# Kernel optimization log

Measured on AMD Instinct MI355X. Metric: run time of the kernel, lower is better.

The kernel has to match this reference:

```python
import jax, jax.numpy as jnp
import numpy as np

EMBED_DIM = 1024
NUM_HEADS = 16
HEAD_DIM = EMBED_DIM // NUM_HEADS
B, S = 4, 2048


def setup_inputs() -> dict:
    key = jax.random.key(0)
    ks = jax.random.split(key, 9)
    scale = 1.0 / np.sqrt(EMBED_DIM)
    x = jax.random.normal(ks[0], (B, S, EMBED_DIM), dtype=jnp.float32)
    Wq = jax.random.normal(ks[1], (EMBED_DIM, EMBED_DIM), dtype=jnp.float32) * scale
    Wk = jax.random.normal(ks[2], (EMBED_DIM, EMBED_DIM), dtype=jnp.float32) * scale
    Wv = jax.random.normal(ks[3], (EMBED_DIM, EMBED_DIM), dtype=jnp.float32) * scale
    Wo = jax.random.normal(ks[4], (EMBED_DIM, EMBED_DIM), dtype=jnp.float32) * scale
    bq = jnp.zeros((EMBED_DIM,), jnp.float32)
    bk = jnp.zeros((EMBED_DIM,), jnp.float32)
    bv = jnp.zeros((EMBED_DIM,), jnp.float32)
    bo = jnp.zeros((EMBED_DIM,), jnp.float32)
    return {"x": x, "Wq": Wq, "bq": bq, "Wk": Wk, "bk": bk, "Wv": Wv, "bv": bv, "Wo": Wo, "bo": bo}


def _split_heads(t):
    # [B,S,E] -> [B,H,S,D]
    b, s, _ = t.shape
    return t.reshape(b, s, NUM_HEADS, HEAD_DIM).transpose(0, 2, 1, 3)


def reference(x, Wq, bq, Wk, bk, Wv, bv, Wo, bo):
    q = _split_heads(x @ Wq + bq)
    k = _split_heads(x @ Wk + bk)
    v = _split_heads(x @ Wv + bv)
    scale = 1.0 / jnp.sqrt(jnp.asarray(HEAD_DIM, x.dtype))
    scores = jnp.einsum('bhqd,bhkd->bhqk', q, k) * scale  # [B,H,S,S]
    weights = jax.nn.softmax(scores, axis=-1)
    attn = jnp.einsum('bhqk,bhkd->bhqd', weights, v)  # [B,H,S,D]
    b, h, s, d = attn.shape
    concat = attn.transpose(0, 2, 1, 3).reshape(b, s, h * d)
    return concat @ Wo + bo
```

## Files before the change

### kernel.cpp

```cpp
#include <hip/hip_runtime.h>
#include <hip/hip_bf16.h>

typedef unsigned short u16;
typedef __attribute__((ext_vector_type(8))) short bf16x8;
typedef __attribute__((ext_vector_type(4))) float f32x4;
typedef __attribute__((ext_vector_type(4))) unsigned short u16x4;

#define EMB 1024
#define SEQ 2048
#define NH 16
#define HD 64

#define OFF_WT   0u
#define OFF_WOT  3145728u
#define OFF_Q    4194304u
#define OFF_K    12582912u
#define OFF_VT   20971520u
#define OFF_OC   29360128u

#define QSCALE 0.1803368801111f

__device__ __forceinline__ u16 f2bf(float f) {
    unsigned int x; __builtin_memcpy(&x, &f, 4);
    unsigned int r = x + 0x7fffu + ((x >> 16) & 1u);
    return (u16)(r >> 16);
}

#if defined(__has_builtin) && __has_builtin(__builtin_amdgcn_cvt_pk_bf16_f32)
typedef __attribute__((ext_vector_type(2))) __bf16 bfv2;
__device__ __forceinline__ unsigned int pkbf(float a, float b) {
    bfv2 v = __builtin_amdgcn_cvt_pk_bf16_f32(a, b);
    unsigned int u; __builtin_memcpy(&u, &v, 4); return u;
}
#else
__device__ __forceinline__ unsigned int pkbf(float a, float b) {
    return (unsigned)f2bf(a) | ((unsigned)f2bf(b) << 16);
}
#endif

#if defined(__has_builtin) && __has_builtin(__builtin_amdgcn_exp2f)
__device__ __forceinline__ float exp2fast(float x) { return __builtin_amdgcn_exp2f(x); }
#else
__device__ __forceinline__ float exp2fast(float x) { return __builtin_exp2f(x); }
#endif

__device__ __forceinline__ void gld_lds16(const void* gsrc, void* ldst) {
    void* g = const_cast<void*>(gsrc);
    __builtin_amdgcn_global_load_lds((__attribute__((address_space(1))) void*)g,
                                     (__attribute__((address_space(3))) void*)ldst,
                                     16, 0, 0);
}

__global__ __launch_bounds__(256) void convert_x(
    const float* __restrict__ x, u16* __restrict__ xb)
{
    int i = (blockIdx.x * 256 + threadIdx.x) * 4;
    float4 v = *(const float4*)&x[i];
    uint2 o = { pkbf(v.x, v.y), pkbf(v.z, v.w) };
    *(uint2*)&xb[i] = o;
}

__global__ __launch_bounds__(256) void transpose_w(
    const float* __restrict__ W0, const float* __restrict__ W1,
    const float* __restrict__ W2, const float* __restrict__ W3,
    u16* __restrict__ ws)
{
    __shared__ u16 tile[64 * 65];
    const float* src = blockIdx.z == 0 ? W0 : blockIdx.z == 1 ? W1 : blockIdx.z == 2 ? W2 : W3;
    u16* dst = ws + (blockIdx.z < 3 ? (unsigned)blockIdx.z * 1048576u : OFF_WOT);
    const int k0 = blockIdx.x * 64, n0 = blockIdx.y * 64;
    const int t = threadIdx.x;
    #pragma unroll
    for (int i = 0; i < 16; i++) {
        int idx = i * 256 + t; int r = idx >> 6, c = idx & 63;
        tile[c * 65 + r] = f2bf(src[(k0 + r) * EMB + n0 + c]);
    }
    __syncthreads();
    #pragma unroll
    for (int i = 0; i < 16; i++) {
        int idx = i * 256 + t; int r = idx >> 6, c = idx & 63;
        dst[(n0 + r) * EMB + k0 + c] = tile[r * 65 + c];
    }
}

__global__ __launch_bounds__(256) void gemm_qkv(
    const u16* __restrict__ X, const u16* __restrict__ WT,
    const float* __restrict__ bq, const float* __restrict__ bk, const float* __restrict__ bv,
    u16* __restrict__ Qt, u16* __restrict__ Ko, u16* __restrict__ Vt)
{
    __shared__ u16 Al[128 * 32];
    __shared__ u16 Bl[128 * 32];
    const int t = threadIdx.x, lane = t & 63, w = t >> 6;
    const int quad = lane >> 4, l15 = lane & 15;
    const int wr = w >> 1, wc = w & 1;
    const int m0 = blockIdx.x * 128, n0 = blockIdx.y * 128;
    const f32x4 fzero = {0.f, 0.f, 0.f, 0.f};

    f32x4 acc[4][4];
    #pragma unroll
    for (int i = 0; i < 4; i++)
        #pragma unroll
        for (int j = 0; j < 4; j++) acc[i][j] = fzero;

    for (int kt = 0; kt < 32; ++kt) {
        #pragma unroll
        for (int r = 0; r < 2; r++) {
            int g = r * 256 + t; int row = g >> 2, cw = g & 3;
            int sc = (cw ^ ((row >> 1) & 3)) * 8;
            gld_lds16(X  + (size_t)(m0 + row) * EMB + kt * 32 + sc, &Al[g * 8]);
            gld_lds16(WT + (size_t)(n0 + row) * EMB + kt * 32 + sc, &Bl[g * 8]);
        }
        __syncthreads();
        bf16x8 af[4], bfr[4];
        #pragma unroll
        for (int i = 0; i < 4; i++) {
            int rowA = wr * 64 + i * 16 + l15;
            af[i] = *(const bf16x8*)&Al[rowA * 32 + ((quad ^ ((rowA >> 1) & 3)) * 8)];
        }
        #pragma unroll
        for (int j = 0; j < 4; j++) {
            int rowB = wc * 64 + j * 16 + l15;
            bfr[j] = *(const bf16x8*)&Bl[rowB * 32 + ((quad ^ ((rowB >> 1) & 3)) * 8)];
        }
        #pragma unroll
        for (int i = 0; i < 4; i++)
            #pragma unroll
            for (int j = 0; j < 4; j++)
                acc[i][j] = __builtin_amdgcn_mfma_f32_16x16x32_bf16(af[i], bfr[j], acc[i][j], 0, 0, 0);
        __syncthreads();
    }

    const int seg = n0 >> 10;
    const float* bias = seg == 0 ? bq : (seg == 1 ? bk : bv);
    #pragma unroll
    for (int j = 0; j < 4; j++) {
        int n = n0 + wc * 64 + j * 16 + l15;
        int nn = n & 1023;
        float bvl = bias[nn];
        int h = nn >> 6, d = nn & 63;
        #pragma unroll
        for (int i = 0; i < 4; i++) {
            int m = m0 + wr * 64 + i * 16 + quad * 4;
            int b = m >> 11, s = m & 2047;
            if (seg == 0) {
                uint2 pp = { pkbf((acc[i][j][0] + bvl) * QSCALE, (acc[i][j][1] + bvl) * QSCALE),
                             pkbf((acc[i][j][2] + bvl) * QSCALE, (acc[i][j][3] + bvl) * QSCALE) };
                *(uint2*)&Qt[(size_t)((b * NH + h) * HD + d) * SEQ + s] = pp;
            } else if (seg == 2) {
                uint2 pp = { pkbf(acc[i][j][0] + bvl, acc[i][j][1] + bvl),
                             pkbf(acc[i][j][2] + bvl, acc[i][j][3] + bvl) };
                *(uint2*)&Vt[(size_t)((b * NH + h) * HD + d) * SEQ + s] = pp;
            } else {
                size_t base = (size_t)((b * NH + h) * SEQ + s) * HD + d;
                #pragma unroll
                for (int r = 0; r < 4; r++) Ko[base + (size_t)r * HD] = f2bf(acc[i][j][r] + bvl);
            }
        }
    }
}

__global__ __launch_bounds__(256, 2) void flash_attn(
    const u16* __restrict__ Q, const u16* __restrict__ K,
    const u16* __restrict__ VT, u16* __restrict__ Oc)
{
    __shared__ u16 Kl[64 * 64];
    __shared__ u16 Vl[64 * 64];
    __shared__ u16 Pl[4 * 64 * 72];
    const int t = threadIdx.x, lane = t & 63, w = t >> 6;
    const int quad = lane >> 4, l15 = lane & 15;
    const int a7 = l15 & 7;
    const int bh = blockIdx.y;
    const int b = bh >> 4, h = bh & 15;
    const int q0 = blockIdx.x * 256 + w * 64;
    const u16* Qtb = Q + (size_t)bh * HD * SEQ;
    const u16* Kb  = K + (size_t)bh * SEQ * HD;
    const u16* Vb  = VT + (size_t)bh * HD * SEQ;
    const f32x4 fzero = {0.f, 0.f, 0.f, 0.f};

    const u16* kbase0 = &Kl[l15 * 64 + ((quad ^ a7) * 8)];
    const u16* kbase1 = &Kl[l15 * 64 + (((4 + quad) ^ a7) * 8)];
    const u16* vbase0 = &Vl[l15 * 64 + ((quad ^ a7) * 8)];
    const u16* vbase1 = &Vl[l15 * 64 + (((4 + quad) ^ a7) * 8)];
    u16* Pw = &Pl[w * 64 * 72];
    u16* pww = Pw + l15 * 72 + quad * 4;
    const u16* pwr = Pw + l15 * 72 + quad * 8;

    bf16x8 ones;
    #pragma unroll
    for (int j = 0; j < 8; j++) ones[j] = (short)0x3F80;

    bf16x8 qf[4][2];
    #pragma unroll
    for (int i = 0; i < 4; i++)
        #pragma unroll
        for (int c = 0; c < 2; c++)
            #pragma unroll
            for (int j = 0; j < 8; j++)
                qf[i][c][j] = (short)Qtb[(size_t)(c * 32 + quad * 8 + j) * SEQ + q0 + i * 16 + l15];

    f32x4 oacc[4][4];
    f32x4 oextra[4];
    #pragma unroll
    for (int i = 0; i < 4; i++) {
        oextra[i] = fzero;
        #pragma unroll
        for (int f = 0; f < 4; f++) oacc[i][f] = fzero;
    }

    for (int kt = 0; kt < 32; ++kt) {
        #pragma unroll
        for (int r = 0; r < 2; r++) {
            int g = r * 256 + t, row = g >> 3, cw = g & 7;
            int swz = (cw ^ (row & 7)) * 8;
            gld_lds16(Kb + (size_t)kt * 64 * HD + row * HD + swz, &Kl[g * 8]);
            gld_lds16(Vb + (size_t)row * SEQ + kt * 64 + swz, &Vl[g * 8]);
        }
        __syncthreads();

        {
            bf16x8 ak[2][4];
            #pragma unroll
            for (int f = 0; f < 4; f++) {
                ak[0][f] = *(const bf16x8*)(kbase0 + f * 1024);
                ak[1][f] = *(const bf16x8*)(kbase1 + f * 1024);
            }
            #pragma unroll
            for (int i = 0; i < 4; i++) {
                f32x4 sf[4];
                #pragma unroll
                for (int f = 0; f < 4; f++) sf[f] = fzero;
                #pragma unroll
                for (int c = 0; c < 2; c++)
                    #pragma unroll
                    for (int f = 0; f < 4; f++)
                        sf[f] = __builtin_amdgcn_mfma_f32_16x16x32_bf16(ak[c][f], qf[i][c], sf[f], 0, 0, 0);
                #pragma unroll
                for (int f = 0; f < 4; f++) {
                    float p0 = exp2fast(sf[f][0]);
                    float p1 = exp2fast(sf[f][1]);
                    float p2 = exp2fast(sf[f][2]);
                    float p3 = exp2fast(sf[f][3]);
                    uint2 pp = { pkbf(p0, p1), pkbf(p2, p3) };
                    *(uint2*)(pww + i * 1152 + f * 16) = pp;
                }
            }
        }

        {
            bf16x8 av[2][4];
            #pragma unroll
            for (int f = 0; f < 4; f++) {
                av[0][f] = *(const bf16x8*)(vbase0 + f * 1024);
                av[1][f] = *(const bf16x8*)(vbase1 + f * 1024);
            }
            #pragma unroll
            for (int i = 0; i < 4; i++) {
                bf16x8 bp0 = *(const bf16x8*)(pwr + i * 1152);
                bf16x8 bp1 = *(const bf16x8*)(pwr + i * 1152 + 32);
                #pragma unroll
                for (int f = 0; f < 4; f++) {
                    oacc[i][f] = __builtin_amdgcn_mfma_f32_16x16x32_bf16(av[0][f], bp0, oacc[i][f], 0, 0, 0);
                    oacc[i][f] = __builtin_amdgcn_mfma_f32_16x16x32_bf16(av[1][f], bp1, oacc[i][f], 0, 0, 0);
                }
                oextra[i] = __builtin_amdgcn_mfma_f32_16x16x32_bf16(ones, bp0, oextra[i], 0, 0, 0);
                oextra[i] = __builtin_amdgcn_mfma_f32_16x16x32_bf16(ones, bp1, oextra[i], 0, 0, 0);
            }
        }
        __syncthreads();
    }

    #pragma unroll
    for (int i = 0; i < 4; i++) {
        float inv = 1.0f / oextra[i][0];
        int s = q0 + i * 16 + l15;
        size_t base = ((size_t)(b * SEQ + s) * NH + h) * HD;
        #pragma unroll
        for (int f = 0; f < 4; f++) {
            uint2 o = { pkbf(oacc[i][f][0] * inv, oacc[i][f][1] * inv),
                        pkbf(oacc[i][f][2] * inv, oacc[i][f][3] * inv) };
            *(uint2*)&Oc[base + f * 16 + quad * 4] = o;
        }
    }
}

__global__ __launch_bounds__(256) void gemm_out(
    const u16* __restrict__ A, const u16* __restrict__ WT,
    const float* __restrict__ bo, float* __restrict__ out)
{
    __shared__ u16 Al[128 * 32];
    __shared__ u16 Bl[128 * 32];
    const int t = threadIdx.x, lane = t & 63, w = t >> 6;
    const int quad = lane >> 4, l15 = lane & 15;
    const int wr = w >> 1, wc = w & 1;
    const int m0 = blockIdx.x * 128, n0 = blockIdx.y * 128;
    const f32x4 fzero = {0.f, 0.f, 0.f, 0.f};

    f32x4 acc[4][4];
    #pragma unroll
    for (int i = 0; i < 4; i++)
        #pragma unroll
        for (int j = 0; j < 4; j++) acc[i][j] = fzero;

    for (int kt = 0; kt < 32; ++kt) {
        #pragma unroll
        for (int r = 0; r < 2; r++) {
            int g = r * 256 + t; int row = g >> 2, cw = g & 3;
            int sc = (cw ^ ((row >> 1) & 3)) * 8;
            gld_lds16(A  + (size_t)(m0 + row) * EMB + kt * 32 + sc, &Al[g * 8]);
            gld_lds16(WT + (size_t)(n0 + row) * EMB + kt * 32 + sc, &Bl[g * 8]);
        }
        __syncthreads();
        bf16x8 af[4], bfr[4];
        #pragma unroll
        for (int i = 0; i < 4; i++) {
            int rowA = wr * 64 + i * 16 + l15;
            af[i] = *(const bf16x8*)&Al[rowA * 32 + ((quad ^ ((rowA >> 1) & 3)) * 8)];
        }
        #pragma unroll
        for (int j = 0; j < 4; j++) {
            int rowB = wc * 64 + j * 16 + l15;
            bfr[j] = *(const bf16x8*)&Bl[rowB * 32 + ((quad ^ ((rowB >> 1) & 3)) * 8)];
        }
        #pragma unroll
        for (int i = 0; i < 4; i++)
            #pragma unroll
            for (int j = 0; j < 4; j++)
                acc[i][j] = __builtin_amdgcn_mfma_f32_16x16x32_bf16(af[i], bfr[j], acc[i][j], 0, 0, 0);
        __syncthreads();
    }

    #pragma unroll
    for (int j = 0; j < 4; j++) {
        int n = n0 + wc * 64 + j * 16 + l15;
        float bvl = bo[n];
        #pragma unroll
        for (int i = 0; i < 4; i++) {
            int m = m0 + wr * 64 + i * 16 + quad * 4;
            #pragma unroll
            for (int r = 0; r < 4; r++)
                out[(size_t)(m + r) * EMB + n] = acc[i][j][r] + bvl;
        }
    }
}

extern "C" void kernel_launch(void* const* d_in, const int* in_sizes, int n_in,
                              void* d_out, int out_size, void* d_ws, size_t ws_size,
                              hipStream_t stream)
{
    (void)in_sizes; (void)n_in; (void)out_size; (void)ws_size;
    const float* x  = (const float*)d_in[0];
    const float* Wq = (const float*)d_in[1];
    const float* bq = (const float*)d_in[2];
    const float* Wk = (const float*)d_in[3];
    const float* bk = (const float*)d_in[4];
    const float* Wv = (const float*)d_in[5];
    const float* bv = (const float*)d_in[6];
    const float* Wo = (const float*)d_in[7];
    const float* bo = (const float*)d_in[8];
    u16* ws = (u16*)d_ws;
    u16* Xb = (u16*)d_out;

    convert_x<<<dim3(8192), 256, 0, stream>>>(x, Xb);
    transpose_w<<<dim3(16, 16, 4), 256, 0, stream>>>(Wq, Wk, Wv, Wo, ws);
    gemm_qkv<<<dim3(64, 24), 256, 0, stream>>>(Xb, ws + OFF_WT, bq, bk, bv,
                                               ws + OFF_Q, ws + OFF_K, ws + OFF_VT);
    flash_attn<<<dim3(8, 64), 256, 0, stream>>>(ws + OFF_Q, ws + OFF_K,
                                                ws + OFF_VT, ws + OFF_OC);
    gemm_out<<<dim3(64, 8), 256, 0, stream>>>(ws + OFF_OC, ws + OFF_WOT, bo, (float*)d_out);
}
```

Measured before the change: 292.6 us.

## Double-buffer K/V tiles and interleave QK/PV per row block in flash attention

The flash attention loop now prefetches the next K/V tile into a second LDS buffer while computing on the current one. It uses a single barrier per iteration instead of loading and then syncing. The QK^T, exp and PV steps are fused per 16-row block, with a small P scratch buffer that alternates by parity, and s_setprio raises wave priority around the MFMA groups. This is meant to hide global-load latency and cut LDS footprint. In exchange it needs more registers, since av and ak are both live, and LDS use for K/V doubles.

Result: no change. 295.9 us (+1.1%).

```diff
diff --git a/kernel.cpp b/kernel.cpp
--- a/kernel.cpp
+++ b/kernel.cpp
@@ -163,9 +163,9 @@
     const u16* __restrict__ Q, const u16* __restrict__ K,
     const u16* __restrict__ VT, u16* __restrict__ Oc)
 {
-    __shared__ u16 Kl[64 * 64];
-    __shared__ u16 Vl[64 * 64];
-    __shared__ u16 Pl[4 * 64 * 72];
+    __shared__ u16 Kl[2][64 * 64];
+    __shared__ u16 Vl[2][64 * 64];
+    __shared__ u16 Pl[4][2][16 * 72];
     const int t = threadIdx.x, lane = t & 63, w = t >> 6;
     const int quad = lane >> 4, l15 = lane & 15;
     const int a7 = l15 & 7;
@@ -177,13 +177,10 @@
     const u16* Vb  = VT + (size_t)bh * HD * SEQ;
     const f32x4 fzero = {0.f, 0.f, 0.f, 0.f};
 
-    const u16* kbase0 = &Kl[l15 * 64 + ((quad ^ a7) * 8)];
-    const u16* kbase1 = &Kl[l15 * 64 + (((4 + quad) ^ a7) * 8)];
-    const u16* vbase0 = &Vl[l15 * 64 + ((quad ^ a7) * 8)];
-    const u16* vbase1 = &Vl[l15 * 64 + (((4 + quad) ^ a7) * 8)];
-    u16* Pw = &Pl[w * 64 * 72];
-    u16* pww = Pw + l15 * 72 + quad * 4;
-    const u16* pwr = Pw + l15 * 72 + quad * 8;
+    const int kf0 = l15 * 64 + ((quad ^ a7) * 8);
+    const int kf1 = l15 * 64 + (((4 + quad) ^ a7) * 8);
+    u16* pww = &Pl[w][0][l15 * 72 + quad * 4];
+    const u16* pwr = &Pl[w][0][l15 * 72 + quad * 8];
 
     bf16x8 ones;
     #pragma unroll
@@ -207,66 +204,79 @@
         for (int f = 0; f < 4; f++) oacc[i][f] = fzero;
     }
 
-    for (int kt = 0; kt < 32; ++kt) {
+    auto stage = [&](int kt, int bsel) {
         #pragma unroll
         for (int r = 0; r < 2; r++) {
             int g = r * 256 + t, row = g >> 3, cw = g & 7;
             int swz = (cw ^ (row & 7)) * 8;
-            gld_lds16(Kb + (size_t)kt * 64 * HD + row * HD + swz, &Kl[g * 8]);
-            gld_lds16(Vb + (size_t)row * SEQ + kt * 64 + swz, &Vl[g * 8]);
-        }
-        __syncthreads();
-
-        {
-            bf16x8 ak[2][4];
+            gld_lds16(Kb + (size_t)kt * 64 * HD + row * HD + swz, &Kl[bsel][g * 8]);
+            gld_lds16(Vb + (size_t)row * SEQ + kt * 64 + swz, &Vl[bsel][g * 8]);
+        }
+    };
+
+    stage(0, 0);
+    asm volatile("s_waitcnt vmcnt(0) lgkmcnt(0)" ::: "memory");
+    __builtin_amdgcn_s_barrier();
+    __builtin_amdgcn_sched_barrier(0);
+
+    int cur = 0;
+    for (int kt = 0; kt < 32; ++kt) {
+        if (kt < 31) stage(kt + 1, cur ^ 1);
+
+        const u16* kbuf = &Kl[cur][0];
+        const u16* vbuf = &Vl[cur][0];
+        bf16x8 ak[2][4], av[2][4];
+        #pragma unroll
+        for (int f = 0; f < 4; f++) {
+            ak[0][f] = *(const bf16x8*)(kbuf + kf0 + f * 1024);
+            ak[1][f] = *(const bf16x8*)(kbuf + kf1 + f * 1024);
+            av[0][f] = *(const bf16x8*)(vbuf + kf0 + f * 1024);
+            av[1][f] = *(const bf16x8*)(vbuf + kf1 + f * 1024);
+        }
+
+        #pragma unroll
+        for (int i = 0; i < 4; i++) {
+            const int par = (i & 1) * 1152;
+            f32x4 sf[4];
+            #pragma unroll
+            for (int f = 0; f < 4; f++) sf[f] = fzero;
+            __builtin_amdgcn_s_setprio(1);
+            #pragma unroll
+            for (int c = 0; c < 2; c++)
+                #pragma unroll
+                for (int f = 0; f < 4; f++)
+                    sf[f] = __builtin_amdgcn_mfma_f32_16x16x32_bf16(ak[c][f], qf[i][c], sf[f], 0, 0, 0);
+            __builtin_amdgcn_s_setprio(0);
+
             #pragma unroll
             for (int f = 0; f < 4; f++) {
-                ak[0][f] = *(const bf16x8*)(kbase0 + f * 1024);
-                ak[1][f] = *(const bf16x8*)(kbase1 + f * 1024);
+                float p0 = exp2fast(sf[f][0]);
+                float p1 = exp2fast(sf[f][1]);
+                float p2 = exp2fast(sf[f][2]);
+                float p3 = exp2fast(sf[f][3]);
+                uint2 pp = { pkbf(p0, p1), pkbf(p2, p3) };
+                *(uint2*)(pww + par + f * 16) = pp;
             }
-            #pragma unroll
-            for (int i = 0; i < 4; i++) {
-                f32x4 sf[4];
-                #pragma unroll
-                for (int f = 0; f < 4; f++) sf[f] = fzero;
-                #pragma unroll
-                for (int c = 0; c < 2; c++)
-                    #pragma unroll
-                    for (int f = 0; f < 4; f++)
-                        sf[f] = __builtin_amdgcn_mfma_f32_16x16x32_bf16(ak[c][f], qf[i][c], sf[f], 0, 0, 0);
-                #pragma unroll
-                for (int f = 0; f < 4; f++) {
-                    float p0 = exp2fast(sf[f][0]);
-                    float p1 = exp2fast(sf[f][1]);
-                    float p2 = exp2fast(sf[f][2]);
-                    float p3 = exp2fast(sf[f][3]);
-                    uint2 pp = { pkbf(p0, p1), pkbf(p2, p3) };
-                    *(uint2*)(pww + i * 1152 + f * 16) = pp;
-                }
+            bf16x8 bp0 = *(const bf16x8*)(pwr + par);
+            bf16x8 bp1 = *(const bf16x8*)(pwr + par + 32);
+
+            __builtin_amdgcn_s_setprio(1);
+            #pragma unroll
+            for (int f = 0; f < 4; f++) {
+                oacc[i][f] = __builtin_amdgcn_mfma_f32_16x16x32_bf16(av[0][f], bp0, oacc[i][f], 0, 0, 0);
+                oacc[i][f] = __builtin_amdgcn_mfma_f32_16x16x32_bf16(av[1][f], bp1, oacc[i][f], 0, 0, 0);
             }
-        }
-
-        {
-            bf16x8 av[2][4];
-            #pragma unroll
-            for (int f = 0; f < 4; f++) {
-                av[0][f] = *(const bf16x8*)(vbase0 + f * 1024);
-                av[1][f] = *(const bf16x8*)(vbase1 + f * 1024);
-            }
-            #pragma unroll
-            for (int i = 0; i < 4; i++) {
-                bf16x8 bp0 = *(const bf16x8*)(pwr + i * 1152);
-                bf16x8 bp1 = *(const bf16x8*)(pwr + i * 1152 + 32);
-                #pragma unroll
-                for (int f = 0; f < 4; f++) {
-                    oacc[i][f] = __builtin_amdgcn_mfma_f32_16x16x32_bf16(av[0][f], bp0, oacc[i][f], 0, 0, 0);
-                    oacc[i][f] = __builtin_amdgcn_mfma_f32_16x16x32_bf16(av[1][f], bp1, oacc[i][f], 0, 0, 0);
-                }
-                oextra[i] = __builtin_amdgcn_mfma_f32_16x16x32_bf16(ones, bp0, oextra[i], 0, 0, 0);
-                oextra[i] = __builtin_amdgcn_mfma_f32_16x16x32_bf16(ones, bp1, oextra[i], 0, 0, 0);
-            }
-        }
-        __syncthreads();
+            oextra[i] = __builtin_amdgcn_mfma_f32_16x16x32_bf16(ones, bp0, oextra[i], 0, 0, 0);
+            oextra[i] = __builtin_amdgcn_mfma_f32_16x16x32_bf16(ones, bp1, oextra[i], 0, 0, 0);
+            __builtin_amdgcn_s_setprio(0);
+        }
+
+        if (kt < 31) {
+            asm volatile("s_waitcnt vmcnt(0) lgkmcnt(0)" ::: "memory");
+            __builtin_amdgcn_s_barrier();
+            __builtin_amdgcn_sched_barrier(0);
+        }
+        cur ^= 1;
     }
 
     #pragma unroll
```
